# Optimization experiments

Measured on AMD Instinct MI355X. Metric: run time of the kernel, lower is better.

Reference implementation:

```python
import jax, jax.numpy as jnp
from jax import lax
import numpy as np

NBITS = 3  # PartialSumLSQ bit width


def binarize(x):
    # straight-through sign (Binarize in BNN code modifies .data -> identity STE)
    return x + lax.stop_gradient(jnp.sign(x) - x)


def lsq(y, alpha):
    # LSQ quantizer for partial sums: q = round(clamp(y/a, Qn, Qp)) * a, STE round,
    # gradient-scaled step size (forward value unaffected by g).
    Qn, Qp = -(2 ** (NBITS - 1)), 2 ** (NBITS - 1) - 1
    g = 1.0 / np.sqrt(y.size * Qp)
    a = alpha * g + lax.stop_gradient(alpha - alpha * g)
    yc = jnp.clip(y / a, Qn, Qp)
    yq = yc + lax.stop_gradient(jnp.round(yc) - yc)
    return yq * a


def split_slices(xp, cgroups):
    # xp: [B, 128*cgroups, H+2, W+2]; reproduces split_tensor_128/256/512 ordering:
    # channel group outermost, then col offset j, then row offset i.
    H, W = xp.shape[2] - 2, xp.shape[3] - 2
    sl = [xp[:, g * 128:(g + 1) * 128, i:i + H, j:j + W]
          for g in range(cgroups) for j in range(3) for i in range(3)]
    return jnp.stack(sl)  # [S, B, 128, H, W]


def psum_stage(x, w, b, alpha, cgroups):
    # emulated 3x3 binary conv: pad, split into S shifted 128-ch slices, per-slice
    # binarized 1x1 conv + bias, LSQ-quantize each partial sum, accumulate.
    xp = jnp.pad(binarize(x), ((0, 0), (0, 0), (1, 1), (1, 1)))
    xs = split_slices(xp, cgroups)                      # [S,B,128,H,W]
    y = jnp.einsum('sbchw,soc->sbohw', xs, binarize(w)) + b[:, None, :, None, None]
    return jax.vmap(lsq)(y, alpha).sum(0)               # [B,Cout,H,W]


def maxpool2(x):
    return lax.reduce_window(x, -jnp.inf, lax.max, (1, 1, 2, 2), (1, 1, 2, 2), 'VALID')


def bn(x, g, b):
    # eval-mode BatchNorm with running_mean=0, running_var=1 -> affine
    s = (1, -1) + (1,) * (x.ndim - 2)
    return x * g.reshape(s) + b.reshape(s)


def htanh(x):
    return jnp.clip(x, -1.0, 1.0)


def _forward(x, conv1_w, conv1_b, s2_w, s2_b, s2_a, s3_w, s3_b, s3_a,
             s4_w, s4_b, s4_a, s5_w, s5_b, s5_a, s6_w, s6_b, s6_a,
             bn1_g, bn1_b, bn2_g, bn2_b, bn3_g, bn3_b, bn4_g, bn4_b,
             bn5_g, bn5_b, bn6_g, bn6_b, fc1_w, fc1_b, fc2_w, fc2_b,
             fc3_w, fc3_b, fbn1_g, fbn1_b, fbn2_g, fbn2_b, fbn3_g, fbn3_b):
    # conv1: 3->128 3x3 pad1; input has 3 channels -> not binarized, weight binarized
    h = lax.conv_general_dilated(x, binarize(conv1_w), (1, 1), ((1, 1), (1, 1)),
                                 dimension_numbers=('NCHW', 'OIHW', 'NCHW'))
    h = h + conv1_b[None, :, None, None]
    h = htanh(bn(h, bn1_g, bn1_b))
    h = psum_stage(h, s2_w, s2_b, s2_a, 1)   # 128->128, 9 slices, 32x32
    h = maxpool2(h)                          # 16x16
    h = htanh(bn(h, bn2_g, bn2_b))
    h = psum_stage(h, s3_w, s3_b, s3_a, 1)   # 128->256, 9 slices
    h = htanh(bn(h, bn3_g, bn3_b))
    h = psum_stage(h, s4_w, s4_b, s4_a, 2)   # 256->256, 18 slices
    h = maxpool2(h)                          # 8x8
    h = htanh(bn(h, bn4_g, bn4_b))
    h = psum_stage(h, s5_w, s5_b, s5_a, 2)   # 256->512, 18 slices
    h = htanh(bn(h, bn5_g, bn5_b))
    h = psum_stage(h, s6_w, s6_b, s6_a, 4)   # 512->512, 36 slices
    h = maxpool2(h)                          # 4x4
    h = htanh(bn(h, bn6_g, bn6_b))
    # binarized classifier: 512*4*4 -> 1024 -> 1024 -> num_classes
    f = binarize(h.reshape(h.shape[0], -1))
    f = f @ binarize(fc1_w).T + fc1_b
    f = htanh(f * fbn1_g + fbn1_b)
    f = binarize(f) @ binarize(fc2_w).T + fc2_b
    f = htanh(f * fbn2_g + fbn2_b)
    f = binarize(f) @ binarize(fc3_w).T + fc3_b
    return f * fbn3_g + fbn3_b


def setup_inputs() -> dict:
    key = jax.random.key(0)
    ks = iter(jax.random.split(key, 80))
    def rn(shape, scale=1.0):
        return jax.random.normal(next(ks), shape, jnp.float32) * scale
    d = {}
    d['x'] = rn((64, 3, 32, 32))
    d['conv1_w'] = rn((128, 3, 3, 3), 0.1)
    d['conv1_b'] = rn((128,), 0.01)
    stages = {'s2': (9, 128), 's3': (9, 256), 's4': (18, 256),
              's5': (18, 512), 's6': (36, 512)}
    for name, (S, co) in stages.items():
        d[name + '_w'] = rn((S, co, 128), 0.1)
        d[name + '_b'] = rn((S, co), 0.01)
        d[name + '_a'] = jax.random.uniform(next(ks), (S,), jnp.float32, 0.05, 0.15)
    for i, c in zip(range(1, 7), [128, 128, 256, 256, 512, 512]):
        d[f'bn{i}_g'] = jnp.ones((c,), jnp.float32) + rn((c,), 0.01)
        d[f'bn{i}_b'] = rn((c,), 0.01)
    d['fc1_w'] = rn((1024, 512 * 16), 0.02); d['fc1_b'] = rn((1024,), 0.01)
    d['fc2_w'] = rn((1024, 1024), 0.02);     d['fc2_b'] = rn((1024,), 0.01)
    d['fc3_w'] = rn((10, 1024), 0.02);       d['fc3_b'] = rn((10,), 0.01)
    for i, c in zip(range(1, 4), [1024, 1024, 10]):
        d[f'fbn{i}_g'] = jnp.ones((c,), jnp.float32) + rn((c,), 0.01)
        d[f'fbn{i}_b'] = rn((c,), 0.01)
    return d


def reference(x, conv1_w, conv1_b, s2_w, s2_b, s2_a, s3_w, s3_b, s3_a,
              s4_w, s4_b, s4_a, s5_w, s5_b, s5_a, s6_w, s6_b, s6_a,
              bn1_g, bn1_b, bn2_g, bn2_b, bn3_g, bn3_b, bn4_g, bn4_b,
              bn5_g, bn5_b, bn6_g, bn6_b, fc1_w, fc1_b, fc2_w, fc2_b,
              fc3_w, fc3_b, fbn1_g, fbn1_b, fbn2_g, fbn2_b, fbn3_g, fbn3_b):
    return _forward(x, conv1_w, conv1_b, s2_w, s2_b, s2_a, s3_w, s3_b, s3_a,
                    s4_w, s4_b, s4_a, s5_w, s5_b, s5_a, s6_w, s6_b, s6_a,
                    bn1_g, bn1_b, bn2_g, bn2_b, bn3_g, bn3_b, bn4_g, bn4_b,
                    bn5_g, bn5_b, bn6_g, bn6_b, fc1_w, fc1_b, fc2_w, fc2_b,
                    fc3_w, fc3_b, fbn1_g, fbn1_b, fbn2_g, fbn2_b, fbn3_g, fbn3_b)
```

## Files before the change

### kernel.cpp

```cpp
#include <hip/hip_runtime.h>
#include <hip/hip_bf16.h>
#include <math.h>

typedef unsigned long long u64;

struct PrepArgs {
    const float* w[7];
    u64* out[7];
    int cnt[7];
    int mode[7];
    const float* fc1w;
    u64* fc1T;
    const float* alpha[5];
    const float* bias[5];
    int loff[5];
    int lCout[5];
    double gq[5];
    u64* wlut;
    double* czv;
    int czoff[5];
    int czS[5];
    int R1, R2, R3, R4;
};

__global__ __launch_bounds__(256)
void k_prep(PrepArgs A) {
    int gid = blockIdx.x * 256 + threadIdx.x;
    int lane = threadIdx.x & 63;
    if (gid < A.R1) {
        int wid = gid >> 6;
        int seg = 0, base = 0, pre = 0;
#pragma unroll
        for (int t = 0; t < 7; ++t) {
            if (wid >= pre) { seg = t; base = pre; }
            pre += A.cnt[t];
        }
        int li = wid - base;
        const float* p = A.w[seg] + ((size_t)li << 6);
        u64 m = __ballot(p[lane] > 0.f);
        if (lane == 0) {
            int mode = A.mode[seg];
            size_t idx = (mode == 1) ? ((size_t)(li >> 1) * 4 + (li & 1))
                       : (mode == 2) ? ((size_t)(li & 15) * 1024 + (li >> 4))
                       : (size_t)li;
            A.out[seg][idx] = m;
        }
    } else if (gid < A.R2) {
        int wid = (gid - A.R1) >> 6;
        int row = wid >> 3, gk = wid & 7;
        int g = gk >> 1, k = gk & 1;
        int c = g * 128 + k * 64 + lane;
        const float* p = A.fc1w + (size_t)row * 8192 + (size_t)c * 16;
        float arr[16];
#pragma unroll
        for (int q = 0; q < 4; ++q) {
            float4 f = ((const float4*)p)[q];
            arr[4 * q + 0] = f.x; arr[4 * q + 1] = f.y;
            arr[4 * q + 2] = f.z; arr[4 * q + 3] = f.w;
        }
#pragma unroll
        for (int h = 0; h < 4; ++h)
#pragma unroll
        for (int xq = 0; xq < 4; ++xq) {
            u64 m = __ballot(arr[h * 4 + xq] > 0.f);
            if (lane == 0) {
                int wd = g * 32 + h * 8 + xq * 2 + k;
                A.fc1T[(size_t)wd * 1024 + row] = m;
            }
        }
    } else if (gid < A.R3) {
        int idx = gid - A.R2;
        int seg = 0;
#pragma unroll
        for (int t = 1; t < 5; ++t) if (idx >= A.loff[t]) seg = t;
        int li = idx - A.loff[seg];
        int s = li / A.lCout[seg];
        double al = (double)A.alpha[seg][s];
        double tg = al * A.gq[seg];
        double a  = tg + (al - tg);
        double b  = (double)A.bias[seg][li];
        double q0 = rint(fmin(fmax(b / a, -4.0), 3.0));
        double qp = rint(fmin(fmax((2.0 + b) / a, -4.0), 3.0));
        double qn = rint(fmin(fmax((-2.0 + b) / a, -4.0), 3.0));
        double cz = q0 * a;
        A.wlut[(size_t)idx * 4 + 2] = __double_as_longlong(qp * a - cz);
        A.wlut[(size_t)idx * 4 + 3] = __double_as_longlong(qn * a - cz);
    } else if (gid < A.R4) {
        int idx = gid - A.R3;
        int seg = 0;
#pragma unroll
        for (int t = 1; t < 5; ++t) if (idx >= A.czoff[t]) seg = t;
        int o = idx - A.czoff[seg];
        int Cout = A.lCout[seg];
        double CZ = 0.0;
        for (int s = 0; s < A.czS[seg]; ++s) {
            double al = (double)A.alpha[seg][s];
            double tg = al * A.gq[seg];
            double a  = tg + (al - tg);
            double b  = (double)A.bias[seg][s * Cout + o];
            double q0 = rint(fmin(fmax(b / a, -4.0), 3.0));
            CZ += q0 * a;
        }
        A.czv[idx] = CZ;
    }
}

__global__ __launch_bounds__(128)
void k_conv1(const float* __restrict__ x, const float* __restrict__ w,
             const float* __restrict__ cb, const float* __restrict__ g1,
             const float* __restrict__ b1, u64* __restrict__ apack) {
    __shared__ double xs[3][3][34];
    int h = blockIdx.x & 31;
    int b = blockIdx.x >> 5;
    int tid = threadIdx.x;
    for (int idx = tid; idx < 306; idx += 128) {
        int dyy = idx / 102;
        int rem = idx - dyy * 102;
        int ci = rem / 34;
        int col = rem - ci * 34;
        int y = h + dyy - 1, xx = col - 1;
        double v = 0.0;
        if ((unsigned)y < 32u && (unsigned)xx < 32u)
            v = (double)x[((b * 3 + ci) * 32 + y) * 32 + xx];
        xs[dyy][ci][col] = v;
    }
    __syncthreads();
    int o = tid;
    double sg[3][3][3];
#pragma unroll
    for (int ci = 0; ci < 3; ++ci)
#pragma unroll
    for (int ky = 0; ky < 3; ++ky)
#pragma unroll
    for (int kx = 0; kx < 3; ++kx) {
        float wv = w[o * 27 + (ci * 3 + ky) * 3 + kx];
        sg[kx][ci][ky] = wv > 0.f ? 1.0 : (wv < 0.f ? -1.0 : 0.0);
    }
    double cbv = (double)cb[o], g1v = (double)g1[o], b1v = (double)b1[o];
    double A0 = 0.0, A1 = 0.0, A2 = 0.0;
    for (int pc = 0; pc < 34; ++pc) {
        double v[3][3];
#pragma unroll
        for (int ky = 0; ky < 3; ++ky)
#pragma unroll
        for (int ci = 0; ci < 3; ++ci)
            v[ky][ci] = xs[ky][ci][pc];
        A2 = 0.0;
#pragma unroll
        for (int ci = 0; ci < 3; ++ci)
#pragma unroll
        for (int ky = 0; ky < 3; ++ky) {
            A0 += v[ky][ci] * sg[2][ci][ky];
            A1 += v[ky][ci] * sg[1][ci][ky];
            A2 += v[ky][ci] * sg[0][ci][ky];
        }
        if (pc >= 2) {
            int wc = pc - 2;
            double t = (A0 + cbv) * g1v + b1v;
            u64 m = __ballot(t > 0.0);
            if ((tid & 63) == 0)
                apack[((size_t)(b * 1024 + h * 32 + wc)) * 2 + (tid >> 6)] = m;
        }
        A0 = A1; A1 = A2;
    }
}

template <int POOL, int G, int H, int W, int Cout, int OCH, int NCH, int CWP>
__global__ __launch_bounds__(NCH * OCH)
void k_stage(const u64* __restrict__ apack, const u64* __restrict__ wlut,
             const double* __restrict__ czv,
             const float* __restrict__ gam, const float* __restrict__ bet,
             u64* __restrict__ opack) {
    constexpr int Ho = H / POOL, Wo = W / POOL;
    constexpr int NOC = Cout / OCH;
    constexpr int CRAW = NCH * CWP * POOL;
    constexpr int NROW = POOL + 2;
    constexpr int NCOL = CRAW + 2;
    constexpr int NT = NCH * OCH;
    constexpr int CB = Wo / (NCH * CWP);
    __shared__ alignas(16) u64 sact[G][NROW][NCOL][2];

    int bi = blockIdx.x;
    int oc = bi % NOC; bi /= NOC;
    int cb = bi % CB;  bi /= CB;
    int ph = bi % Ho;
    int b  = bi / Ho;
    int tid = threadIdx.x;
    int ch = tid / OCH;
    int ol = tid - ch * OCH;
    int o  = oc * OCH + ol;
    int colb = cb * CRAW;
    int c0 = colb + ch * CWP * POOL;
    int ybase = ph * POOL - 1;

    for (int t = tid; t < G * NROW * NCOL; t += NT) {
        int g = t / (NROW * NCOL);
        int rr = t - g * (NROW * NCOL);
        int yy = rr / NCOL;
        int xx = rr - yy * NCOL;
        int y = ybase + yy, x = colb - 1 + xx;
        u64 v0 = 0, v1 = 0;
        if ((unsigned)y < (unsigned)H && (unsigned)x < (unsigned)W) {
            const u64* p = apack + (((size_t)((b * G + g) * H + y)) * W + x) * 2;
            v0 = p[0]; v1 = p[1];
        }
        sact[g][yy][xx][0] = v0;
        sact[g][yy][xx][1] = v1;
    }
    __syncthreads();

    double CZ = czv[o];
    double acc[CWP * POOL * POOL];
#pragma unroll
    for (int k = 0; k < CWP * POOL * POOL; ++k) acc[k] = CZ;

    const bool lo0 = (c0 == 0);
    const bool hiW = (c0 + CWP * POOL == W);

#pragma unroll
    for (int g = 0; g < G; ++g) {
#pragma unroll
        for (int j = 0; j < 3; ++j) {
#pragma unroll
            for (int i = 0; i < 3; ++i) {
                const int s = g * 9 + j * 3 + i;
                size_t so = (size_t)s * Cout + o;
                const u64* wl = wlut + so * 4;
                u64 w0 = wl[0], w1 = wl[1];
                double dp = __longlong_as_double(wl[2]);
                double dn = __longlong_as_double(wl[3]);
#pragma unroll
                for (int dy = 0; dy < POOL; ++dy) {
                    int y = ph * POOL + dy + i - 1;
                    if ((unsigned)y >= (unsigned)H) continue;
                    const int yy = dy + i;
#pragma unroll
                    for (int cc = 0; cc < CWP * POOL; ++cc) {
                        if (cc == 0 && j == 0 && lo0) continue;
                        if (cc == CWP * POOL - 1 && j == 2 && hiW) continue;
                        int xx = ch * CWP * POOL + cc + j;
                        u64 a0 = sact[g][yy][xx][0];
                        u64 a1 = sact[g][yy][xx][1];
                        int d = __popcll(a0 ^ w0) + __popcll(a1 ^ w1);
                        double val = (d < 64) ? dp : dn;
                        val = (d == 64) ? 0.0 : val;
                        acc[cc * POOL + dy] += val;
                    }
                }
            }
        }
    }

    double gv = (double)gam[o], bv = (double)bet[o];
#pragma unroll
    for (int cw = 0; cw < CWP; ++cw) {
        double m;
        if constexpr (POOL == 1) {
            m = acc[cw];
        } else {
            m = fmax(fmax(acc[(cw * 2 + 0) * 2 + 0], acc[(cw * 2 + 0) * 2 + 1]),
                     fmax(acc[(cw * 2 + 1) * 2 + 0], acc[(cw * 2 + 1) * 2 + 1]));
        }
        double tt = m * gv + bv;
        u64 bm = __ballot(tt > 0.0);
        if ((tid & 63) == 0) {
            int pw = c0 / POOL + cw;
            opack[(((size_t)(b * (Cout >> 7) + (o >> 7)) * Ho + ph) * Wo + pw) * 2
                  + ((o >> 6) & 1)] = bm;
        }
    }
}

__global__ __launch_bounds__(1024)
void k_fc_all(const u64* __restrict__ abits, const u64* __restrict__ wf1T,
              const float* __restrict__ b1, const float* __restrict__ g1,
              const float* __restrict__ a1,
              const u64* __restrict__ wf2T,
              const float* __restrict__ b2, const float* __restrict__ g2,
              const float* __restrict__ a2,
              const u64* __restrict__ wf3,
              const float* __restrict__ b3, const float* __restrict__ g3,
              const float* __restrict__ a3,
              float* __restrict__ out) {
    __shared__ u64 sa[128];
    __shared__ u64 sp1[16];
    __shared__ u64 sp2[16];
    int b = blockIdx.x;
    int t = threadIdx.x;
    if (t < 128) sa[t] = abits[(size_t)b * 128 + t];
    __syncthreads();
    {
        int d = 0;
#pragma unroll 16
        for (int i = 0; i < 128; ++i)
            d += __popcll(sa[i] ^ wf1T[(size_t)i * 1024 + t]);
        double isum = (double)(8192 - 2 * d);
        double v = (isum + (double)b1[t]) * (double)g1[t] + (double)a1[t];
        u64 m = __ballot(v > 0.0);
        if ((t & 63) == 0) sp1[t >> 6] = m;
    }
    __syncthreads();
    {
        int d = 0;
#pragma unroll
        for (int i = 0; i < 16; ++i)
            d += __popcll(sp1[i] ^ wf2T[(size_t)i * 1024 + t]);
        double isum = (double)(1024 - 2 * d);
        double v = (isum + (double)b2[t]) * (double)g2[t] + (double)a2[t];
        u64 m = __ballot(v > 0.0);
        if ((t & 63) == 0) sp2[t >> 6] = m;
    }
    __syncthreads();
    if (t < 10) {
        int d = 0;
#pragma unroll
        for (int i = 0; i < 16; ++i)
            d += __popcll(sp2[i] ^ wf3[t * 16 + i]);
        double isum = (double)(1024 - 2 * d);
        out[b * 10 + t] = (float)((isum + (double)b3[t]) * (double)g3[t] + (double)a3[t]);
    }
}


extern "C" void kernel_launch(void* const* d_in, const int* in_sizes, int n_in,
                              void* d_out, int out_size, void* d_ws, size_t ws_size,
                              hipStream_t stream) {
    const float* x       = (const float*)d_in[0];
    const float* conv1_w = (const float*)d_in[1];
    const float* conv1_b = (const float*)d_in[2];
    const float* s_w[5]  = {(const float*)d_in[3], (const float*)d_in[6], (const float*)d_in[9],
                            (const float*)d_in[12], (const float*)d_in[15]};
    const float* s_b[5]  = {(const float*)d_in[4], (const float*)d_in[7], (const float*)d_in[10],
                            (const float*)d_in[13], (const float*)d_in[16]};
    const float* s_a[5]  = {(const float*)d_in[5], (const float*)d_in[8], (const float*)d_in[11],
                            (const float*)d_in[14], (const float*)d_in[17]};
    const float* bn_g[6], *bn_b[6];
    for (int i = 0; i < 6; ++i) { bn_g[i] = (const float*)d_in[18 + 2 * i]; bn_b[i] = (const float*)d_in[19 + 2 * i]; }
    const float* fc1_w = (const float*)d_in[30]; const float* fc1_b = (const float*)d_in[31];
    const float* fc2_w = (const float*)d_in[32]; const float* fc2_b = (const float*)d_in[33];
    const float* fc3_w = (const float*)d_in[34]; const float* fc3_b = (const float*)d_in[35];
    const float* fbn_g[3], *fbn_b[3];
    for (int i = 0; i < 3; ++i) { fbn_g[i] = (const float*)d_in[36 + 2 * i]; fbn_b[i] = (const float*)d_in[37 + 2 * i]; }

    size_t off = 0;
    auto alloc = [&](size_t bytes) { off = (off + 255) & ~(size_t)255; size_t o = off; off += bytes; return o; };
    char* ws = (char*)d_ws;
    size_t o_apA  = alloc(1048576);
    size_t o_apB  = alloc(1048576);
    size_t o_wlut = alloc((size_t)35712 * 4 * 8);
    size_t o_cz   = alloc((size_t)1664 * 8);
    size_t o_wf1  = alloc((size_t)1024 * 128 * 8);
    size_t o_wf2  = alloc((size_t)1024 * 16 * 8);
    size_t o_wf3  = alloc((size_t)160 * 8);
    if (off > ws_size) return;

    u64* apA = (u64*)(ws + o_apA);
    u64* apB = (u64*)(ws + o_apB);
    u64* wlut = (u64*)(ws + o_wlut);
    double* czbuf = (double*)(ws + o_cz);
    u64* wf1T = (u64*)(ws + o_wf1);
    u64* wf2T = (u64*)(ws + o_wf2);
    u64* wf3 = (u64*)(ws + o_wf3);

    const int rowoff[5] = {0, 1152, 3456, 8064, 17280};
    const int czoff[5]  = {0, 128, 384, 640, 1152};
    const int sS[5]     = {9, 9, 18, 18, 36};
    const int sCout[5]  = {128, 256, 256, 512, 512};
    const double sYsz[5] = {8388608.0, 4194304.0, 4194304.0, 2097152.0, 2097152.0};

    PrepArgs PA;
    const int scnt[5] = {2304, 4608, 9216, 18432, 36864};
    int totw = 0;
    for (int i = 0; i < 5; ++i) {
        PA.w[i] = s_w[i];
        PA.out[i] = wlut + (size_t)rowoff[i] * 4;
        PA.cnt[i] = scnt[i];
        PA.mode[i] = 1;
        totw += scnt[i];
    }
    PA.w[5] = fc2_w; PA.out[5] = wf2T; PA.cnt[5] = 1024 * 16; PA.mode[5] = 2; totw += 1024 * 16;
    PA.w[6] = fc3_w; PA.out[6] = wf3;  PA.cnt[6] = 160;       PA.mode[6] = 0; totw += 160;
    PA.fc1w = fc1_w; PA.fc1T = wf1T;
    for (int i = 0; i < 5; ++i) {
        PA.alpha[i] = s_a[i]; PA.bias[i] = s_b[i];
        PA.loff[i] = rowoff[i]; PA.lCout[i] = sCout[i];
        PA.gq[i] = 1.0 / sqrt(sYsz[i] * 3.0);
        PA.czoff[i] = czoff[i]; PA.czS[i] = sS[i];
    }
    PA.wlut = wlut; PA.czv = czbuf;
    PA.R1 = totw * 64;
    PA.R2 = PA.R1 + 1024 * 8 * 64;
    PA.R3 = PA.R2 + 35712;
    PA.R4 = PA.R3 + 1664;
    k_prep<<<(PA.R4 + 255) / 256, 256, 0, stream>>>(PA);

    k_conv1<<<64 * 32, 128, 0, stream>>>(x, conv1_w, conv1_b, bn_g[0], bn_b[0], apA);

    k_stage<2, 1, 32, 32, 128, 128, 2, 2><<<64 * 16 * 4 * 1, 256, 0, stream>>>(
        apA, wlut + (size_t)rowoff[0] * 4, czbuf + czoff[0], bn_g[1], bn_b[1], apB);
    k_stage<1, 1, 16, 16, 256, 256, 1, 8><<<64 * 16 * 2 * 1, 256, 0, stream>>>(
        apB, wlut + (size_t)rowoff[1] * 4, czbuf + czoff[1], bn_g[2], bn_b[2], apA);
    k_stage<2, 2, 16, 16, 256, 256, 1, 2><<<64 * 8 * 4 * 1, 256, 0, stream>>>(
        apA, wlut + (size_t)rowoff[2] * 4, czbuf + czoff[2], bn_g[3], bn_b[3], apB);
    k_stage<1, 2, 8, 8, 512, 256, 1, 4><<<64 * 8 * 2 * 2, 256, 0, stream>>>(
        apB, wlut + (size_t)rowoff[3] * 4, czbuf + czoff[3], bn_g[4], bn_b[4], apA);
    k_stage<2, 4, 8, 8, 512, 256, 1, 1><<<64 * 4 * 4 * 2, 256, 0, stream>>>(
        apA, wlut + (size_t)rowoff[4] * 4, czbuf + czoff[4], bn_g[5], bn_b[5], apB);

    k_fc_all<<<64, 1024, 0, stream>>>(apB, wf1T, fc1_b, fbn_g[0], fbn_b[0],
                                      wf2T, fc2_b, fbn_g[1], fbn_b[1],
                                      wf3, fc3_b, fbn_g[2], fbn_b[2],
                                      (float*)d_out);
}
```

Baseline: 221.9 us.

## Restructure binary conv stages to per-row register activation tiles

Rewrites the stage kernel so each wavefront owns 64 output channels and one row segment, loading the three input rows directly from global memory into registers (as 128-bit vectors) instead of staging a tile in shared memory. The max-pool across row pairs is done through a small shared buffer after accumulation, while column pairs are pooled in registers. Launch grids and block sizes are re-derived for every stage. This removes the shared-memory staging and its barrier, and improves reuse of each weight entry across a row. The cost is more register pressure and redundant global activation loads across output-channel blocks.

```diff
diff --git a/kernel.cpp b/kernel.cpp
--- a/kernel.cpp
+++ b/kernel.cpp
@@ -165,108 +165,108 @@
     }
 }
 
-template <int POOL, int G, int H, int W, int Cout, int OCH, int NCH, int CWP>
-__global__ __launch_bounds__(NCH * OCH)
+template <int POOL, int G, int H, int W, int Cout, int RCH, int NCH>
+__global__ __launch_bounds__(64 * RCH * NCH)
 void k_stage(const u64* __restrict__ apack, const u64* __restrict__ wlut,
              const double* __restrict__ czv,
              const float* __restrict__ gam, const float* __restrict__ bet,
              u64* __restrict__ opack) {
+    constexpr int CW = W / NCH;
     constexpr int Ho = H / POOL, Wo = W / POOL;
-    constexpr int NOC = Cout / OCH;
-    constexpr int CRAW = NCH * CWP * POOL;
-    constexpr int NROW = POOL + 2;
-    constexpr int NCOL = CRAW + 2;
-    constexpr int NT = NCH * OCH;
-    constexpr int CB = Wo / (NCH * CWP);
-    __shared__ alignas(16) u64 sact[G][NROW][NCOL][2];
+    constexpr int NOC = Cout / 64;
+    constexpr int NRB = H / RCH;
 
     int bi = blockIdx.x;
-    int oc = bi % NOC; bi /= NOC;
-    int cb = bi % CB;  bi /= CB;
-    int ph = bi % Ho;
-    int b  = bi / Ho;
+    int och = bi % NOC; bi /= NOC;
+    int rb = bi % NRB;
+    int b = bi / NRB;
     int tid = threadIdx.x;
-    int ch = tid / OCH;
-    int ol = tid - ch * OCH;
-    int o  = oc * OCH + ol;
-    int colb = cb * CRAW;
-    int c0 = colb + ch * CWP * POOL;
-    int ybase = ph * POOL - 1;
-
-    for (int t = tid; t < G * NROW * NCOL; t += NT) {
-        int g = t / (NROW * NCOL);
-        int rr = t - g * (NROW * NCOL);
-        int yy = rr / NCOL;
-        int xx = rr - yy * NCOL;
-        int y = ybase + yy, x = colb - 1 + xx;
-        u64 v0 = 0, v1 = 0;
-        if ((unsigned)y < (unsigned)H && (unsigned)x < (unsigned)W) {
-            const u64* p = apack + (((size_t)((b * G + g) * H + y)) * W + x) * 2;
-            v0 = p[0]; v1 = p[1];
-        }
-        sact[g][yy][xx][0] = v0;
-        sact[g][yy][xx][1] = v1;
-    }
-    __syncthreads();
+    int ol = tid & 63;
+    int rr = tid >> 6;
+    int rc = rr / NCH;
+    int nc = rr - rc * NCH;
+    int o = och * 64 + ol;
+    int yr = rb * RCH + rc;
 
     double CZ = czv[o];
-    double acc[CWP * POOL * POOL];
-#pragma unroll
-    for (int k = 0; k < CWP * POOL * POOL; ++k) acc[k] = CZ;
-
-    const bool lo0 = (c0 == 0);
-    const bool hiW = (c0 + CWP * POOL == W);
-
-#pragma unroll
+    double acc[CW];
+#pragma unroll
+    for (int c = 0; c < CW; ++c) acc[c] = CZ;
+
+    ulonglong2 ar[CW + 2];
+
     for (int g = 0; g < G; ++g) {
 #pragma unroll
-        for (int j = 0; j < 3; ++j) {
-#pragma unroll
-            for (int i = 0; i < 3; ++i) {
+        for (int i = 0; i < 3; ++i) {
+            int y = yr + i - 1;
+            if ((unsigned)y >= (unsigned)H) continue;
+            const ulonglong2* rp = (const ulonglong2*)
+                (apack + ((((size_t)(b * G + g) * H + y) * W + nc * CW - 1)) * 2);
+#pragma unroll
+            for (int k = 0; k < CW + 2; ++k) {
+                if ((k > 0 || nc > 0) && (k < CW + 1 || nc < NCH - 1))
+                    ar[k] = rp[k];
+            }
+#pragma unroll
+            for (int j = 0; j < 3; ++j) {
                 const int s = g * 9 + j * 3 + i;
                 size_t so = (size_t)s * Cout + o;
-                const u64* wl = wlut + so * 4;
-                u64 w0 = wl[0], w1 = wl[1];
-                double dp = __longlong_as_double(wl[2]);
-                double dn = __longlong_as_double(wl[3]);
-#pragma unroll
-                for (int dy = 0; dy < POOL; ++dy) {
-                    int y = ph * POOL + dy + i - 1;
-                    if ((unsigned)y >= (unsigned)H) continue;
-                    const int yy = dy + i;
-#pragma unroll
-                    for (int cc = 0; cc < CWP * POOL; ++cc) {
-                        if (cc == 0 && j == 0 && lo0) continue;
-                        if (cc == CWP * POOL - 1 && j == 2 && hiW) continue;
-                        int xx = ch * CWP * POOL + cc + j;
-                        u64 a0 = sact[g][yy][xx][0];
-                        u64 a1 = sact[g][yy][xx][1];
-                        int d = __popcll(a0 ^ w0) + __popcll(a1 ^ w1);
-                        double val = (d < 64) ? dp : dn;
-                        val = (d == 64) ? 0.0 : val;
-                        acc[cc * POOL + dy] += val;
-                    }
+                ulonglong2 wv = *(const ulonglong2*)(wlut + so * 4);
+                ulonglong2 dv = *(const ulonglong2*)(wlut + so * 4 + 2);
+                u64 w0 = wv.x, w1 = wv.y;
+                double dp = __longlong_as_double(dv.x);
+                double dn = __longlong_as_double(dv.y);
+#pragma unroll
+                for (int c = 0; c < CW; ++c) {
+                    if (c == 0 && j == 0 && nc == 0) continue;
+                    if (c == CW - 1 && j == 2 && nc == NCH - 1) continue;
+                    u64 a0 = ar[c + j].x, a1 = ar[c + j].y;
+                    int d = __popcll(a0 ^ w0) + __popcll(a1 ^ w1);
+                    double val = (d < 64) ? dp : dn;
+                    val = (d == 64) ? 0.0 : val;
+                    acc[c] += val;
                 }
             }
         }
     }
 
     double gv = (double)gam[o], bv = (double)bet[o];
-#pragma unroll
-    for (int cw = 0; cw < CWP; ++cw) {
-        double m;
-        if constexpr (POOL == 1) {
-            m = acc[cw];
-        } else {
-            m = fmax(fmax(acc[(cw * 2 + 0) * 2 + 0], acc[(cw * 2 + 0) * 2 + 1]),
-                     fmax(acc[(cw * 2 + 1) * 2 + 0], acc[(cw * 2 + 1) * 2 + 1]));
-        }
-        double tt = m * gv + bv;
-        u64 bm = __ballot(tt > 0.0);
-        if ((tid & 63) == 0) {
-            int pw = c0 / POOL + cw;
-            opack[(((size_t)(b * (Cout >> 7) + (o >> 7)) * Ho + ph) * Wo + pw) * 2
-                  + ((o >> 6) & 1)] = bm;
+    if constexpr (POOL == 1) {
+#pragma unroll
+        for (int c = 0; c < CW; ++c) {
+            double t = acc[c] * gv + bv;
+            u64 bm = __ballot(t > 0.0);
+            if (ol == 0) {
+                int pw = nc * CW + c;
+                opack[(((size_t)(b * (Cout >> 7) + (o >> 7)) * Ho + yr) * Wo + pw) * 2
+                      + (och & 1)] = bm;
+            }
+        }
+    } else {
+        __shared__ double pl[RCH / 2][NCH][CW / 2][64];
+        double m2[CW / 2];
+#pragma unroll
+        for (int c2 = 0; c2 < CW / 2; ++c2)
+            m2[c2] = fmax(acc[2 * c2], acc[2 * c2 + 1]);
+        if (rc & 1) {
+#pragma unroll
+            for (int c2 = 0; c2 < CW / 2; ++c2)
+                pl[rc >> 1][nc][c2][ol] = m2[c2];
+        }
+        __syncthreads();
+        if (!(rc & 1)) {
+#pragma unroll
+            for (int c2 = 0; c2 < CW / 2; ++c2) {
+                double m = fmax(m2[c2], pl[rc >> 1][nc][c2][ol]);
+                double t = m * gv + bv;
+                u64 bm = __ballot(t > 0.0);
+                if (ol == 0) {
+                    int ph = yr >> 1;
+                    int pw = ((nc * CW) >> 1) + c2;
+                    opack[(((size_t)(b * (Cout >> 7) + (o >> 7)) * Ho + ph) * Wo + pw) * 2
+                          + (och & 1)] = bm;
+                }
+            }
         }
     }
 }
@@ -396,15 +396,15 @@
 
     k_conv1<<<64 * 32, 128, 0, stream>>>(x, conv1_w, conv1_b, bn_g[0], bn_b[0], apA);
 
-    k_stage<2, 1, 32, 32, 128, 128, 2, 2><<<64 * 16 * 4 * 1, 256, 0, stream>>>(
+    k_stage<2, 1, 32, 32, 128, 2, 4><<<64 * 16 * 2, 512, 0, stream>>>(
         apA, wlut + (size_t)rowoff[0] * 4, czbuf + czoff[0], bn_g[1], bn_b[1], apB);
-    k_stage<1, 1, 16, 16, 256, 256, 1, 8><<<64 * 16 * 2 * 1, 256, 0, stream>>>(
+    k_stage<1, 1, 16, 16, 256, 2, 2><<<64 * 8 * 4, 256, 0, stream>>>(
         apB, wlut + (size_t)rowoff[1] * 4, czbuf + czoff[1], bn_g[2], bn_b[2], apA);
-    k_stage<2, 2, 16, 16, 256, 256, 1, 2><<<64 * 8 * 4 * 1, 256, 0, stream>>>(
+    k_stage<2, 2, 16, 16, 256, 2, 2><<<64 * 8 * 4, 256, 0, stream>>>(
         apA, wlut + (size_t)rowoff[2] * 4, czbuf + czoff[2], bn_g[3], bn_b[3], apB);
-    k_stage<1, 2, 8, 8, 512, 256, 1, 4><<<64 * 8 * 2 * 2, 256, 0, stream>>>(
+    k_stage<1, 2, 8, 8, 512, 2, 1><<<64 * 4 * 8, 128, 0, stream>>>(
         apB, wlut + (size_t)rowoff[3] * 4, czbuf + czoff[3], bn_g[4], bn_b[4], apA);
-    k_stage<2, 4, 8, 8, 512, 256, 1, 1><<<64 * 4 * 4 * 2, 256, 0, stream>>>(
+    k_stage<2, 4, 8, 8, 512, 2, 1><<<64 * 4 * 8, 128, 0, stream>>>(
         apA, wlut + (size_t)rowoff[4] * 4, czbuf + czoff[4], bn_g[5], bn_b[5], apB);
 
     k_fc_all<<<64, 1024, 0, stream>>>(apB, wf1T, fc1_b, fbn_g[0], fbn_b[0],
```

Result: slower. 226.7 us (+2.2%).

## Use bf16 MFMA for pooled binary conv stages with pre-swizzled weight fragments

Applied to the files above, without the earlier changes.

The three max-pooled stages (2, 4, 6) move from the bit-packed vector kernel to a new MFMA kernel. It expands packed activations into ±1 bf16 tiles in XOR-swizzled shared memory and computes each slice's 128-channel dot product with 16x16x32 bf16 MFMAs. The sign of each result selects a per-slice quantized LUT value, and the values are accumulated in double. The prep kernel also writes ±1 bf16 weight fragments in MFMA layout. The aim is to replace popcount-style scalar work with matrix cores, at the cost of extra shared-memory expansion and a larger prep pass. The renamed vector kernel's launch bound also changes from NCH*OCH to POOL*OCH, which is harmless for the remaining POOL=1 stages.

```diff
diff --git a/kernel.cpp b/kernel.cpp
--- a/kernel.cpp
+++ b/kernel.cpp
@@ -3,6 +3,8 @@
 #include <math.h>
 
 typedef unsigned long long u64;
+typedef short short8v __attribute__((ext_vector_type(8)));
+typedef float f32x4 __attribute__((ext_vector_type(4)));
 
 struct PrepArgs {
     const float* w[7];
@@ -20,7 +22,12 @@
     double* czv;
     int czoff[5];
     int czS[5];
-    int R1, R2, R3, R4;
+    const float* msw[3];
+    ushort* mwbf[3];
+    int mCout[3];
+    int mS[3];
+    int mtoff[3];
+    int R1, R2, R3, R4, R5;
 };
 
 __global__ __launch_bounds__(256)
@@ -102,6 +109,33 @@
             CZ += q0 * a;
         }
         A.czv[idx] = CZ;
+    } else if (gid < A.R5) {
+        int t = gid - A.R4;
+        int ms = 0;
+#pragma unroll
+        for (int t2 = 1; t2 < 3; ++t2) if (t >= A.mtoff[t2]) ms = t2;
+        int lt = t - A.mtoff[ms];
+        int ln = lt & 63;
+        int fi = lt >> 6;
+        int kc = fi & 3;
+        int rest = fi >> 2;
+        int Cs = A.mCout[ms];
+        int NOCb = Cs >> 4;
+        int oc = rest % NOCb;
+        int s = rest / NOCb;
+        int o = oc * 16 + (ln & 15);
+        int kb = kc * 32 + (ln >> 4) * 8;
+        const float* wp = A.msw[ms] + ((size_t)s * Cs + o) * 128 + kb;
+        u64 lo = 0, hi = 0;
+#pragma unroll
+        for (int e = 0; e < 4; ++e) {
+            u64 v0 = (wp[e] > 0.f) ? 0x3F80ull : 0xBF80ull;
+            u64 v1 = (wp[4 + e] > 0.f) ? 0x3F80ull : 0xBF80ull;
+            lo |= v0 << (16 * e);
+            hi |= v1 << (16 * e);
+        }
+        ulonglong2 st; st.x = lo; st.y = hi;
+        *(ulonglong2*)(A.mwbf[ms] + (size_t)lt * 8) = st;
     }
 }
 
@@ -166,17 +200,17 @@
 }
 
 template <int POOL, int G, int H, int W, int Cout, int OCH, int NCH, int CWP>
-__global__ __launch_bounds__(NCH * OCH)
-void k_stage(const u64* __restrict__ apack, const u64* __restrict__ wlut,
-             const double* __restrict__ czv,
-             const float* __restrict__ gam, const float* __restrict__ bet,
-             u64* __restrict__ opack) {
+__global__ __launch_bounds__(POOL * OCH)
+void k_stage_v(const u64* __restrict__ apack, const u64* __restrict__ wlut,
+               const double* __restrict__ czv,
+               const float* __restrict__ gam, const float* __restrict__ bet,
+               u64* __restrict__ opack) {
     constexpr int Ho = H / POOL, Wo = W / POOL;
     constexpr int NOC = Cout / OCH;
     constexpr int CRAW = NCH * CWP * POOL;
     constexpr int NROW = POOL + 2;
     constexpr int NCOL = CRAW + 2;
-    constexpr int NT = NCH * OCH;
+    constexpr int NT = POOL * OCH;
     constexpr int CB = Wo / (NCH * CWP);
     __shared__ alignas(16) u64 sact[G][NROW][NCOL][2];
 
@@ -267,6 +301,144 @@
             int pw = c0 / POOL + cw;
             opack[(((size_t)(b * (Cout >> 7) + (o >> 7)) * Ho + ph) * Wo + pw) * 2
                   + ((o >> 6) & 1)] = bm;
+        }
+    }
+}
+
+template <int G, int H, int W, int Cout>
+__global__ __launch_bounds__(512)
+void k_stage_m(const u64* __restrict__ apack, const ushort* __restrict__ wbf,
+               const u64* __restrict__ wlut, const double* __restrict__ czv,
+               const float* __restrict__ gam, const float* __restrict__ bet,
+               u64* __restrict__ opack) {
+    constexpr int NOCb = Cout / 16;
+    constexpr int OGRPS = Cout / 128;
+    constexpr int STRIPS = W / 8;
+    constexpr int TASKS = STRIPS * 8;
+    constexpr int TPW = TASKS / 8;
+    constexpr int BANDS = H / 2;
+    constexpr int WP2 = W + 2;
+    constexpr int PIX = W / 2;
+    constexpr int Ho = H / 2, Wo = W / 2;
+
+    __shared__ alignas(16) ushort img[G][4][WP2][128];
+    __shared__ alignas(16) unsigned char sgn[PIX][128];
+
+    int bi = blockIdx.x;
+    int ogrp = bi % OGRPS; bi /= OGRPS;
+    int band = bi % BANDS;
+    int b = bi / BANDS;
+    int tid = threadIdx.x;
+    int lane = tid & 63;
+    int wid = tid >> 6;
+
+    for (int cell = tid; cell < G * 4 * WP2; cell += 512) {
+        int g = cell / (4 * WP2);
+        int r2 = cell - g * (4 * WP2);
+        int yy = r2 / WP2;
+        int xx = r2 - yy * WP2;
+        int y = band * 2 + yy - 1;
+        int xg = xx - 1;
+        u64 a0 = 0, a1 = 0;
+        bool ok = ((unsigned)y < (unsigned)H) && ((unsigned)xg < (unsigned)W);
+        if (ok) {
+            const u64* p = apack + ((size_t)((b * G + g) * H + y) * W + xg) * 2;
+            a0 = p[0]; a1 = p[1];
+        }
+        char* cp = (char*)&img[g][yy][xx][0];
+        int sw8 = (xx & 7) << 3;
+#pragma unroll
+        for (int p2 = 0; p2 < 32; ++p2) {
+            unsigned lo = ok ? ((unsigned)((a0 >> (2 * p2)) & 1) ? 0x3F80u : 0xBF80u) : 0u;
+            unsigned hi = ok ? ((unsigned)((a0 >> (2 * p2 + 1)) & 1) ? 0x3F80u : 0xBF80u) : 0u;
+            *(unsigned*)(cp + (((2 * p2) ^ sw8) * 2)) = lo | (hi << 16);
+        }
+#pragma unroll
+        for (int p2 = 0; p2 < 32; ++p2) {
+            unsigned lo = ok ? ((unsigned)((a1 >> (2 * p2)) & 1) ? 0x3F80u : 0xBF80u) : 0u;
+            unsigned hi = ok ? ((unsigned)((a1 >> (2 * p2 + 1)) & 1) ? 0x3F80u : 0xBF80u) : 0u;
+            *(unsigned*)(cp + (((64 + 2 * p2) ^ sw8) * 2)) = lo | (hi << 16);
+        }
+    }
+    __syncthreads();
+
+#pragma unroll 1
+    for (int tt = 0; tt < TPW; ++tt) {
+        int task = wid * TPW + tt;
+        int oc_l = task & 7;
+        int strip = task >> 3;
+        int oc = ogrp * 8 + oc_l;
+        int n = lane & 15;
+        int q = lane >> 4;
+        int o = oc * 16 + n;
+        int r = n >> 3;
+        int cx = n & 7;
+
+        double CZ = czv[o];
+        double acc0 = CZ, acc1 = CZ, acc2 = CZ, acc3 = CZ;
+
+#pragma unroll 1
+        for (int g = 0; g < G; ++g) {
+#pragma unroll
+            for (int j = 0; j < 3; ++j) {
+#pragma unroll
+                for (int i = 0; i < 3; ++i) {
+                    int s = g * 9 + j * 3 + i;
+                    size_t so = (size_t)s * Cout + o;
+                    const ushort* wb = wbf + (((size_t)(s * NOCb + oc) * 4) * 64 + lane) * 8;
+                    short8v b0 = *(const short8v*)(wb);
+                    short8v b1 = *(const short8v*)(wb + 512);
+                    short8v b2 = *(const short8v*)(wb + 1024);
+                    short8v b3 = *(const short8v*)(wb + 1536);
+                    int xx = strip * 8 + cx + j;
+                    const ushort* cp = &img[g][r + i][xx][0];
+                    int sw8 = (xx & 7) << 3;
+                    short8v a0 = *(const short8v*)(cp + ((q * 8) ^ sw8));
+                    short8v a1 = *(const short8v*)(cp + ((32 + q * 8) ^ sw8));
+                    short8v a2 = *(const short8v*)(cp + ((64 + q * 8) ^ sw8));
+                    short8v a3 = *(const short8v*)(cp + ((96 + q * 8) ^ sw8));
+                    f32x4 c = {0.f, 0.f, 0.f, 0.f};
+                    c = __builtin_amdgcn_mfma_f32_16x16x32_bf16(a0, b0, c, 0, 0, 0);
+                    c = __builtin_amdgcn_mfma_f32_16x16x32_bf16(a1, b1, c, 0, 0, 0);
+                    c = __builtin_amdgcn_mfma_f32_16x16x32_bf16(a2, b2, c, 0, 0, 0);
+                    c = __builtin_amdgcn_mfma_f32_16x16x32_bf16(a3, b3, c, 0, 0, 0);
+                    const u64* wl = wlut + so * 4;
+                    double dp = __longlong_as_double(wl[2]);
+                    double dn = __longlong_as_double(wl[3]);
+                    float v0 = c[0], v1 = c[1], v2 = c[2], v3 = c[3];
+                    double t0 = (v0 > 0.f) ? dp : dn; t0 = (v0 == 0.f) ? 0.0 : t0; acc0 += t0;
+                    double t1 = (v1 > 0.f) ? dp : dn; t1 = (v1 == 0.f) ? 0.0 : t1; acc1 += t1;
+                    double t2 = (v2 > 0.f) ? dp : dn; t2 = (v2 == 0.f) ? 0.0 : t2; acc2 += t2;
+                    double t3 = (v3 > 0.f) ? dp : dn; t3 = (v3 == 0.f) ? 0.0 : t3; acc3 += t3;
+                }
+            }
+        }
+
+        double gv = (double)gam[o], bv = (double)bet[o];
+        double m0 = fmax(acc0, __shfl_xor(acc0, 32));
+        double m1 = fmax(acc1, __shfl_xor(acc1, 32));
+        double m2 = fmax(acc2, __shfl_xor(acc2, 32));
+        double m3 = fmax(acc3, __shfl_xor(acc3, 32));
+        if (q < 2) {
+            double p0 = fmax(m0, m1);
+            double p1 = fmax(m2, m3);
+            int pw = strip * 4 + (q & 1) * 2;
+            sgn[pw + 0][oc_l * 16 + n] = (p0 * gv + bv > 0.0) ? 1 : 0;
+            sgn[pw + 1][oc_l * 16 + n] = (p1 * gv + bv > 0.0) ? 1 : 0;
+        }
+    }
+    __syncthreads();
+
+    constexpr int WORDS = PIX * 2;
+    for (int wt = wid; wt < WORDS; wt += 8) {
+        int pix = wt >> 1;
+        int wl = wt & 1;
+        u64 bm = __ballot(sgn[pix][wl * 64 + lane] != 0);
+        if (lane == 0) {
+            int o_g = ogrp * 128 + wl * 64;
+            int gout = o_g >> 7;
+            int wsel = (o_g >> 6) & 1;
+            opack[(((size_t)(b * (Cout >> 7) + gout) * Ho + band) * Wo + pix) * 2 + wsel] = bm;
         }
     }
 }
@@ -352,6 +524,9 @@
     size_t o_wf1  = alloc((size_t)1024 * 128 * 8);
     size_t o_wf2  = alloc((size_t)1024 * 16 * 8);
     size_t o_wf3  = alloc((size_t)160 * 8);
+    const int fragcnt[3] = {288, 1152, 4608};
+    size_t o_wbf[3];
+    for (int i = 0; i < 3; ++i) o_wbf[i] = alloc((size_t)fragcnt[i] * 1024);
     if (off > ws_size) return;
 
     u64* apA = (u64*)(ws + o_apA);
@@ -361,6 +536,8 @@
     u64* wf1T = (u64*)(ws + o_wf1);
     u64* wf2T = (u64*)(ws + o_wf2);
     u64* wf3 = (u64*)(ws + o_wf3);
+    ushort* wbf[3];
+    for (int i = 0; i < 3; ++i) wbf[i] = (ushort*)(ws + o_wbf[i]);
 
     const int rowoff[5] = {0, 1152, 3456, 8064, 17280};
     const int czoff[5]  = {0, 128, 384, 640, 1152};
@@ -388,24 +565,35 @@
         PA.czoff[i] = czoff[i]; PA.czS[i] = sS[i];
     }
     PA.wlut = wlut; PA.czv = czbuf;
+    const int msidx[3] = {0, 2, 4};
+    int mpre = 0;
+    for (int i = 0; i < 3; ++i) {
+        PA.msw[i] = s_w[msidx[i]];
+        PA.mwbf[i] = wbf[i];
+        PA.mCout[i] = sCout[msidx[i]];
+        PA.mS[i] = sS[msidx[i]];
+        PA.mtoff[i] = mpre;
+        mpre += fragcnt[i] * 64;
+    }
     PA.R1 = totw * 64;
     PA.R2 = PA.R1 + 1024 * 8 * 64;
     PA.R3 = PA.R2 + 35712;
     PA.R4 = PA.R3 + 1664;
-    k_prep<<<(PA.R4 + 255) / 256, 256, 0, stream>>>(PA);
+    PA.R5 = PA.R4 + mpre;
+    k_prep<<<(PA.R5 + 255) / 256, 256, 0, stream>>>(PA);
 
     k_conv1<<<64 * 32, 128, 0, stream>>>(x, conv1_w, conv1_b, bn_g[0], bn_b[0], apA);
 
-    k_stage<2, 1, 32, 32, 128, 128, 2, 2><<<64 * 16 * 4 * 1, 256, 0, stream>>>(
-        apA, wlut + (size_t)rowoff[0] * 4, czbuf + czoff[0], bn_g[1], bn_b[1], apB);
-    k_stage<1, 1, 16, 16, 256, 256, 1, 8><<<64 * 16 * 2 * 1, 256, 0, stream>>>(
+    k_stage_m<1, 32, 32, 128><<<64 * 16 * 1, 512, 0, stream>>>(
+        apA, wbf[0], wlut + (size_t)rowoff[0] * 4, czbuf + czoff[0], bn_g[1], bn_b[1], apB);
+    k_stage_v<1, 1, 16, 16, 256, 256, 1, 8><<<64 * 16 * 2, 256, 0, stream>>>(
         apB, wlut + (size_t)rowoff[1] * 4, czbuf + czoff[1], bn_g[2], bn_b[2], apA);
-    k_stage<2, 2, 16, 16, 256, 256, 1, 2><<<64 * 8 * 4 * 1, 256, 0, stream>>>(
-        apA, wlut + (size_t)rowoff[2] * 4, czbuf + czoff[2], bn_g[3], bn_b[3], apB);
-    k_stage<1, 2, 8, 8, 512, 256, 1, 4><<<64 * 8 * 2 * 2, 256, 0, stream>>>(
+    k_stage_m<2, 16, 16, 256><<<64 * 8 * 2, 512, 0, stream>>>(
+        apA, wbf[1], wlut + (size_t)rowoff[2] * 4, czbuf + czoff[2], bn_g[3], bn_b[3], apB);
+    k_stage_v<1, 2, 8, 8, 512, 256, 1, 4><<<64 * 8 * 2 * 2, 256, 0, stream>>>(
         apB, wlut + (size_t)rowoff[3] * 4, czbuf + czoff[3], bn_g[4], bn_b[4], apA);
-    k_stage<2, 4, 8, 8, 512, 256, 1, 1><<<64 * 4 * 4 * 2, 256, 0, stream>>>(
-        apA, wlut + (size_t)rowoff[4] * 4, czbuf + czoff[4], bn_g[5], bn_b[5], apB);
+    k_stage_m<4, 8, 8, 512><<<64 * 4 * 4, 512, 0, stream>>>(
+        apA, wbf[2], wlut + (size_t)rowoff[4] * 4, czbuf + czoff[4], bn_g[5], bn_b[5], apB);
 
     k_fc_all<<<64, 1024, 0, stream>>>(apB, wf1T, fc1_b, fbn_g[0], fbn_b[0],
                                       wf2T, fc2_b, fbn_g[1], fbn_b[1],
```

Result: slower. 359.6 us (+62.1%).
